# Performance work log

Hardware: AMD Instinct MI355X
Metric: run time of the kernel (lower is better)

The kernel has to match this reference:

```python
import jax, jax.numpy as jnp
import numpy as np

ATTWSIZE = 64  # sliding window length (matches init_kwargs attwsize)


def setup_inputs() -> dict:
    key = jax.random.key(0)
    k1, k2, k3 = jax.random.split(key, 3)
    B, T, D, A = 32, 4096, 256, 128
    x = jax.random.normal(k1, (B, T, D), dtype=jnp.float32)
    Wp = jax.random.normal(k2, (A, D), dtype=jnp.float32) / np.sqrt(D).astype(np.float32)
    bp = jnp.zeros((A,), dtype=jnp.float32)
    Wg = jax.random.normal(k3, (1, A), dtype=jnp.float32) / np.sqrt(A).astype(np.float32)
    return {"x": x, "Wp": Wp, "bp": bp, "Wg": Wg}


def _windowed_sum(v, w):
    # causal sliding-window sum over axis=1: sum(v[:, max(t-w+1,0):t+1, :])
    # single-pass cumsum formulation: cs[t] - cs[t-w]
    cs = jnp.cumsum(v, axis=1)
    T = v.shape[1]
    shifted = jnp.pad(cs, ((0, 0), (w, 0), (0, 0)))[:, :T, :]
    return cs - shifted


def reference(x, Wp, bp, Wg):
    # proj = tanh(Linear(dimio->dimatt)(x))
    proj = jnp.tanh(jnp.einsum('btd,ad->bta', x, Wp) + bp)
    # gvec = sigmoid(Linear(dimatt->1, no bias)(proj))  -> [B, T, 1]
    g = jax.nn.sigmoid(jnp.einsum('bta,oa->bto', proj, Wg))
    wx = g * x  # gated input [B, T, D]
    num = _windowed_sum(wx, ATTWSIZE)         # [B, T, D]
    den = _windowed_sum(g, ATTWSIZE)          # [B, T, 1] broadcasts over D
    return num / den
```

## Files before the change

### kernel.cpp

```cpp
#include <hip/hip_runtime.h>

#define TT 4096
#define DD 256
#define AA 128
#define WIN 64

typedef short bf16x8 __attribute__((ext_vector_type(8)));
typedef float f32x4 __attribute__((ext_vector_type(4)));

__device__ __forceinline__ unsigned short f2bf(float f) {
    unsigned int u = __builtin_bit_cast(unsigned int, f);
    u += 0x7FFFu + ((u >> 16) & 1u);
    return (unsigned short)(u >> 16);
}

__global__ __launch_bounds__(256) void prep_wp(const float* __restrict__ Wp,
                                               unsigned short* __restrict__ wpb) {
    int i = blockIdx.x * 256 + threadIdx.x;
    wpb[i] = f2bf(Wp[i]);
}

#define ROWS 64
#define LDK 264

__global__ __launch_bounds__(256) void gate_kernel(
        const float* __restrict__ x, const unsigned short* __restrict__ wpb,
        const float* __restrict__ bp, const float* __restrict__ Wg,
        float* __restrict__ g) {
    __shared__ unsigned short xs[ROWS * LDK];
    const int tid = threadIdx.x;
    const long row0 = (long)blockIdx.x * ROWS;

#pragma unroll
    for (int it = 0; it < 16; ++it) {
        int idx = it * 256 + tid;
        int r   = idx >> 6;
        int c4  = idx & 63;
        float4 v = reinterpret_cast<const float4*>(x + (row0 + r) * DD)[c4];
        ushort4 h;
        h.x = f2bf(v.x); h.y = f2bf(v.y); h.z = f2bf(v.z); h.w = f2bf(v.w);
        *reinterpret_cast<ushort4*>(&xs[r * LDK + c4 * 4]) = h;
    }
    __syncthreads();

    const int lane = tid & 63;
    const int wave = tid >> 6;
    const int quad = lane >> 4;
    const int nrow = lane & 15;

    f32x4 acc[8];
#pragma unroll
    for (int nt = 0; nt < 8; ++nt) acc[nt] = (f32x4){0.f, 0.f, 0.f, 0.f};

    const unsigned short* xbase = &xs[(wave * 16 + nrow) * LDK + quad * 8];
#pragma unroll
    for (int k0 = 0; k0 < 8; ++k0) {
        bf16x8 afrag = *reinterpret_cast<const bf16x8*>(xbase + k0 * 32);
#pragma unroll
        for (int nt = 0; nt < 8; ++nt) {
            bf16x8 bfrag = *reinterpret_cast<const bf16x8*>(
                wpb + (nt * 16 + nrow) * DD + k0 * 32 + quad * 8);
            acc[nt] = __builtin_amdgcn_mfma_f32_16x16x32_bf16(afrag, bfrag, acc[nt], 0, 0, 0);
        }
    }

    float rowsum[4] = {0.f, 0.f, 0.f, 0.f};
#pragma unroll
    for (int nt = 0; nt < 8; ++nt) {
        int n = nt * 16 + nrow;
        float wg = Wg[n];
        float bv = bp[n];
#pragma unroll
        for (int r = 0; r < 4; ++r) {
            float pre = acc[nt][r] + bv;
            float e = __expf(2.0f * pre);
            float th = 1.0f - 2.0f / (e + 1.0f);
            rowsum[r] += th * wg;
        }
    }
#pragma unroll
    for (int off = 1; off <= 8; off <<= 1) {
#pragma unroll
        for (int r = 0; r < 4; ++r)
            rowsum[r] += __shfl_xor(rowsum[r], off, 64);
    }
    if (nrow == 0) {
#pragma unroll
        for (int r = 0; r < 4; ++r) {
            long row = row0 + wave * 16 + quad * 4 + r;
            float s = rowsum[r];
            g[row] = 1.0f / (1.0f + __expf(-s));
        }
    }
}

__global__ __launch_bounds__(256) void den_kernel(const float* __restrict__ g,
                                                  float* __restrict__ invden) {
    int idx = blockIdx.x * 256 + threadIdx.x;
    int t = idx & (TT - 1);
    const float* gb = g + (idx - t);
    int lo = t - (WIN - 1); if (lo < 0) lo = 0;
    float s = 0.f;
    for (int u = lo; u <= t; ++u) s += gb[u];
    invden[idx] = 1.0f / s;
}

#define TC 256
#define NCHUNK 16

__global__ __launch_bounds__(256) void stream_kernel(
        const float* __restrict__ x, const float* __restrict__ g,
        const float* __restrict__ invden, float* __restrict__ out) {
    __shared__ float ring[WIN][DD];
    const int b = blockIdx.x >> 4;
    const int chunk = blockIdx.x & (NCHUNK - 1);
    const int t0 = chunk * TC;
    const int d = threadIdx.x;
    const float* xb = x + (size_t)b * TT * DD;
    const float* gb = g + (size_t)b * TT;
    const float* ivb = invden + (size_t)b * TT;
    float* ob = out + (size_t)b * TT * DD;

    float S = 0.f;
#pragma unroll 8
    for (int i = 0; i < WIN; ++i) {
        int s = t0 - WIN + i;
        float v = 0.f;
        if (s >= 0) v = gb[s] * xb[(size_t)s * DD + d];
        ring[i][d] = v;
        S += v;
    }
#pragma unroll 8
    for (int tt = 0; tt < TC; ++tt) {
        int t = t0 + tt;
        int i = tt & (WIN - 1);
        float v = gb[t] * xb[(size_t)t * DD + d];
        S += v - ring[i][d];
        ring[i][d] = v;
        ob[(size_t)t * DD + d] = S * ivb[t];
    }
}

extern "C" void kernel_launch(void* const* d_in, const int* in_sizes, int n_in,
                              void* d_out, int out_size, void* d_ws, size_t ws_size,
                              hipStream_t stream) {
    const float* x  = (const float*)d_in[0];
    const float* Wp = (const float*)d_in[1];
    const float* bp = (const float*)d_in[2];
    const float* Wg = (const float*)d_in[3];
    float* out = (float*)d_out;

    unsigned short* wpb = (unsigned short*)d_ws;
    float* g      = (float*)((char*)d_ws + 65536);
    float* invden = (float*)((char*)d_ws + 65536 + 524288);

    prep_wp<<<AA * DD / 256, 256, 0, stream>>>(Wp, wpb);
    gate_kernel<<<32 * TT / ROWS, 256, 0, stream>>>(x, wpb, bp, Wg, g);
    den_kernel<<<32 * TT / 256, 256, 0, stream>>>(g, invden);
    stream_kernel<<<32 * NCHUNK, 256, 0, stream>>>(x, g, invden, out);
}
```

Before: 317.1 us.

## Restructure gate GEMM with register-resident weights and fuse denominator into stream kernel

The gate kernel now has each wave keep its 32-column slice of the bf16 projection weights in registers and loop over two 64-row subtiles per block, reducing per-wave partial sums through shared memory. The separate denominator kernel is removed: the stream kernel stages the gate values in shared memory, keeps a running sum of gates alongside the running weighted sum, and re-reads the outgoing x row instead of holding it in a shared-memory ring. Stream chunks are halved to raise the block count, and divisions become hardware reciprocals. This removes a launch and the invden round trip, at the cost of extra global reads of x (served by cache) and slightly lower reciprocal precision.

```diff
diff --git a/kernel.cpp b/kernel.cpp
--- a/kernel.cpp
+++ b/kernel.cpp
@@ -20,124 +20,152 @@
     wpb[i] = f2bf(Wp[i]);
 }
 
-#define ROWS 64
 #define LDK 264
+#define RTILE 128
+#define NSUB 2
 
-__global__ __launch_bounds__(256) void gate_kernel(
+__global__ __launch_bounds__(256, 3) void gate_kernel(
         const float* __restrict__ x, const unsigned short* __restrict__ wpb,
         const float* __restrict__ bp, const float* __restrict__ Wg,
         float* __restrict__ g) {
-    __shared__ unsigned short xs[ROWS * LDK];
-    const int tid = threadIdx.x;
-    const long row0 = (long)blockIdx.x * ROWS;
-
-#pragma unroll
-    for (int it = 0; it < 16; ++it) {
-        int idx = it * 256 + tid;
-        int r   = idx >> 6;
-        int c4  = idx & 63;
-        float4 v = reinterpret_cast<const float4*>(x + (row0 + r) * DD)[c4];
-        ushort4 h;
-        h.x = f2bf(v.x); h.y = f2bf(v.y); h.z = f2bf(v.z); h.w = f2bf(v.w);
-        *reinterpret_cast<ushort4*>(&xs[r * LDK + c4 * 4]) = h;
-    }
-    __syncthreads();
-
+    __shared__ unsigned short xs[64 * LDK];
+    __shared__ float psum[4][64];
+    const int tid  = threadIdx.x;
     const int lane = tid & 63;
     const int wave = tid >> 6;
     const int quad = lane >> 4;
     const int nrow = lane & 15;
+    const long row0 = (long)blockIdx.x * RTILE;
 
-    f32x4 acc[8];
+    bf16x8 bfrag[2][8];
+    float bpv[2], wgv[2];
 #pragma unroll
-    for (int nt = 0; nt < 8; ++nt) acc[nt] = (f32x4){0.f, 0.f, 0.f, 0.f};
-
-    const unsigned short* xbase = &xs[(wave * 16 + nrow) * LDK + quad * 8];
+    for (int nt = 0; nt < 2; ++nt) {
+        int n = wave * 32 + nt * 16 + nrow;
+        bpv[nt] = bp[n];
+        wgv[nt] = Wg[n];
 #pragma unroll
-    for (int k0 = 0; k0 < 8; ++k0) {
-        bf16x8 afrag = *reinterpret_cast<const bf16x8*>(xbase + k0 * 32);
-#pragma unroll
-        for (int nt = 0; nt < 8; ++nt) {
-            bf16x8 bfrag = *reinterpret_cast<const bf16x8*>(
-                wpb + (nt * 16 + nrow) * DD + k0 * 32 + quad * 8);
-            acc[nt] = __builtin_amdgcn_mfma_f32_16x16x32_bf16(afrag, bfrag, acc[nt], 0, 0, 0);
-        }
+        for (int k0 = 0; k0 < 8; ++k0)
+            bfrag[nt][k0] = *reinterpret_cast<const bf16x8*>(
+                wpb + n * DD + k0 * 32 + quad * 8);
     }
 
-    float rowsum[4] = {0.f, 0.f, 0.f, 0.f};
+    for (int s = 0; s < NSUB; ++s) {
+        const float* xsrc = x + (row0 + s * 64) * DD;
 #pragma unroll
-    for (int nt = 0; nt < 8; ++nt) {
-        int n = nt * 16 + nrow;
-        float wg = Wg[n];
-        float bv = bp[n];
+        for (int it = 0; it < 16; ++it) {
+            int idx = it * 256 + tid;
+            int r   = idx >> 6;
+            int c4  = idx & 63;
+            float4 v = reinterpret_cast<const float4*>(xsrc + r * DD)[c4];
+            ushort4 h;
+            h.x = f2bf(v.x); h.y = f2bf(v.y); h.z = f2bf(v.z); h.w = f2bf(v.w);
+            *reinterpret_cast<ushort4*>(&xs[r * LDK + c4 * 4]) = h;
+        }
+        __syncthreads();
+
+        f32x4 acc[4][2];
 #pragma unroll
-        for (int r = 0; r < 4; ++r) {
-            float pre = acc[nt][r] + bv;
-            float e = __expf(2.0f * pre);
-            float th = 1.0f - 2.0f / (e + 1.0f);
-            rowsum[r] += th * wg;
+        for (int mt = 0; mt < 4; ++mt)
+#pragma unroll
+            for (int nt = 0; nt < 2; ++nt)
+                acc[mt][nt] = (f32x4){0.f, 0.f, 0.f, 0.f};
+
+#pragma unroll
+        for (int k0 = 0; k0 < 8; ++k0) {
+#pragma unroll
+            for (int mt = 0; mt < 4; ++mt) {
+                bf16x8 af = *reinterpret_cast<const bf16x8*>(
+                    &xs[(mt * 16 + nrow) * LDK + quad * 8 + k0 * 32]);
+                acc[mt][0] = __builtin_amdgcn_mfma_f32_16x16x32_bf16(af, bfrag[0][k0], acc[mt][0], 0, 0, 0);
+                acc[mt][1] = __builtin_amdgcn_mfma_f32_16x16x32_bf16(af, bfrag[1][k0], acc[mt][1], 0, 0, 0);
+            }
         }
-    }
+
+        float p[4][4];
 #pragma unroll
-    for (int off = 1; off <= 8; off <<= 1) {
+        for (int mt = 0; mt < 4; ++mt)
 #pragma unroll
-        for (int r = 0; r < 4; ++r)
-            rowsum[r] += __shfl_xor(rowsum[r], off, 64);
-    }
-    if (nrow == 0) {
+            for (int r = 0; r < 4; ++r) p[mt][r] = 0.f;
 #pragma unroll
-        for (int r = 0; r < 4; ++r) {
-            long row = row0 + wave * 16 + quad * 4 + r;
-            float s = rowsum[r];
-            g[row] = 1.0f / (1.0f + __expf(-s));
+        for (int nt = 0; nt < 2; ++nt) {
+#pragma unroll
+            for (int mt = 0; mt < 4; ++mt) {
+#pragma unroll
+                for (int r = 0; r < 4; ++r) {
+                    float pre = acc[mt][nt][r] + bpv[nt];
+                    float e  = __expf(2.0f * pre);
+                    float th = 1.0f - 2.0f * __builtin_amdgcn_rcpf(e + 1.0f);
+                    p[mt][r] += th * wgv[nt];
+                }
+            }
         }
+#pragma unroll
+        for (int off = 1; off <= 8; off <<= 1)
+#pragma unroll
+            for (int mt = 0; mt < 4; ++mt)
+#pragma unroll
+                for (int r = 0; r < 4; ++r)
+                    p[mt][r] += __shfl_xor(p[mt][r], off, 64);
+        if (nrow == 0) {
+#pragma unroll
+            for (int mt = 0; mt < 4; ++mt)
+#pragma unroll
+                for (int r = 0; r < 4; ++r)
+                    psum[wave][mt * 16 + quad * 4 + r] = p[mt][r];
+        }
+        __syncthreads();
+        if (tid < 64) {
+            float ssum = psum[0][tid] + psum[1][tid] + psum[2][tid] + psum[3][tid];
+            g[row0 + s * 64 + tid] = __builtin_amdgcn_rcpf(1.0f + __expf(-ssum));
+        }
+        __syncthreads();
     }
 }
 
-__global__ __launch_bounds__(256) void den_kernel(const float* __restrict__ g,
-                                                  float* __restrict__ invden) {
-    int idx = blockIdx.x * 256 + threadIdx.x;
-    int t = idx & (TT - 1);
-    const float* gb = g + (idx - t);
-    int lo = t - (WIN - 1); if (lo < 0) lo = 0;
-    float s = 0.f;
-    for (int u = lo; u <= t; ++u) s += gb[u];
-    invden[idx] = 1.0f / s;
-}
-
-#define TC 256
-#define NCHUNK 16
+#define TC 128
+#define NCHUNK (TT / TC)
 
 __global__ __launch_bounds__(256) void stream_kernel(
         const float* __restrict__ x, const float* __restrict__ g,
-        const float* __restrict__ invden, float* __restrict__ out) {
-    __shared__ float ring[WIN][DD];
-    const int b = blockIdx.x >> 4;
+        float* __restrict__ out) {
+    __shared__ float gbuf[TC + WIN];
+    const int b     = blockIdx.x >> 5;
     const int chunk = blockIdx.x & (NCHUNK - 1);
-    const int t0 = chunk * TC;
-    const int d = threadIdx.x;
+    const int t0    = chunk * TC;
+    const int d     = threadIdx.x;
     const float* xb = x + (size_t)b * TT * DD;
     const float* gb = g + (size_t)b * TT;
-    const float* ivb = invden + (size_t)b * TT;
     float* ob = out + (size_t)b * TT * DD;
 
-    float S = 0.f;
-#pragma unroll 8
+    if (d < TC + WIN) {
+        int s = t0 - WIN + d;
+        gbuf[d] = (s >= 0) ? gb[s] : 0.f;
+    }
+    __syncthreads();
+
+    float S = 0.f, Sg = 0.f;
+#pragma unroll 16
     for (int i = 0; i < WIN; ++i) {
-        int s = t0 - WIN + i;
-        float v = 0.f;
-        if (s >= 0) v = gb[s] * xb[(size_t)s * DD + d];
-        ring[i][d] = v;
-        S += v;
+        int s  = t0 - WIN + i;
+        int sc = s < 0 ? 0 : s;
+        float gv = gbuf[i];
+        S  += gv * xb[(size_t)sc * DD + d];
+        Sg += gv;
     }
+
 #pragma unroll 8
     for (int tt = 0; tt < TC; ++tt) {
-        int t = t0 + tt;
-        int i = tt & (WIN - 1);
-        float v = gb[t] * xb[(size_t)t * DD + d];
-        S += v - ring[i][d];
-        ring[i][d] = v;
-        ob[(size_t)t * DD + d] = S * ivb[t];
+        int t  = t0 + tt;
+        int ts = t - WIN;
+        int tsc = ts < 0 ? 0 : ts;
+        float gnew = gbuf[WIN + tt];
+        float gold = gbuf[tt];
+        float vnew = gnew * xb[(size_t)t * DD + d];
+        float vold = gold * xb[(size_t)tsc * DD + d];
+        S  += vnew - vold;
+        Sg += gnew - gold;
+        ob[(size_t)t * DD + d] = S * __builtin_amdgcn_rcpf(Sg);
     }
 }
 
@@ -151,11 +179,9 @@
     float* out = (float*)d_out;
 
     unsigned short* wpb = (unsigned short*)d_ws;
-    float* g      = (float*)((char*)d_ws + 65536);
-    float* invden = (float*)((char*)d_ws + 65536 + 524288);
+    float* g = (float*)((char*)d_ws + 65536);
 
     prep_wp<<<AA * DD / 256, 256, 0, stream>>>(Wp, wpb);
-    gate_kernel<<<32 * TT / ROWS, 256, 0, stream>>>(x, wpb, bp, Wg, g);
-    den_kernel<<<32 * TT / 256, 256, 0, stream>>>(g, invden);
-    stream_kernel<<<32 * NCHUNK, 256, 0, stream>>>(x, g, invden, out);
+    gate_kernel<<<32 * TT / RTILE, 256, 0, stream>>>(x, wpb, bp, Wg, g);
+    stream_kernel<<<32 * NCHUNK, 256, 0, stream>>>(x, g, out);
 }
```

Result: faster. 310.7 us (-2.0%).
